# Kernel tuning notes

Measured on AMD Instinct MI355X. Metric: run time of the kernel, lower is better.

The kernel has to match this reference:

```python
import jax, jax.numpy as jnp
import numpy as np

EPS = 1e-06


def setup_inputs() -> dict:
    key = jax.random.key(0)
    k1, k2, k3 = jax.random.split(key, 3)
    B, L, S, C = 128, 512, 512, 64
    q = jax.random.normal(k1, (B, L, C), dtype=jnp.float32)
    k = jax.random.normal(k2, (B, S, C), dtype=jnp.float32)
    labels = jax.random.randint(k3, (B, L, S), 0, 2, dtype=jnp.int64)
    return {"q": q, "k": k, "labels": labels}


def reference(q, k, labels):
    # sim: [B, L, S], mapped to (0, 1) via (1 + cos-like sim) / 2
    sim = (1.0 + jnp.einsum('blc,bsc->bls', q, k)) * 0.5

    # column-wise stats (over L) -> [B, S]; torch.std uses ddof=1 (unbiased)
    col = (jnp.max(sim, axis=1) - jnp.mean(sim, axis=1)) / jnp.std(sim, axis=1, ddof=1)
    sharp1 = jax.nn.softmax(col, axis=-1)  # [B, S]

    # row-wise stats (over S) -> [B, L]
    row = (jnp.max(sim, axis=2) - jnp.mean(sim, axis=2)) / jnp.std(sim, axis=2, ddof=1)
    sharp2 = jax.nn.softmax(row, axis=-1)  # [B, L]

    simc = jnp.clip(sim, EPS, 1.0 - EPS)
    nll = -jnp.log(simc)                    # [B, L, S]
    nll_neg = -jnp.log(1.0 - simc)          # [B, L, S]

    pos = (labels == 1).astype(sim.dtype)
    neg = (labels == 0).astype(sim.dtype)

    # masked sums per sample, weighted by sharpness (broadcast over rows/cols)
    loss1 = jnp.sum(nll * sharp1[:, None, :] * pos, axis=(1, 2))  # [B]
    loss2 = jnp.sum(nll * sharp2[:, :, None] * pos, axis=(1, 2))  # [B]
    loss3 = jnp.sum(nll_neg * neg, axis=(1, 2)) / jnp.sum(neg, axis=(1, 2))  # [B]

    losses = (loss1 + loss2) * 0.5 + loss3
    return (sharp1, jnp.mean(losses))
```

## Files before the change

kernel.cpp:

```cpp
#include <hip/hip_runtime.h>

#define EPSF 1e-6f

typedef _Float16 half8 __attribute__((ext_vector_type(8)));
typedef float f32x4 __attribute__((ext_vector_type(4)));

constexpr int B = 128, L = 512, S = 512, C = 64;
constexpr int TILE_R = 64;
constexpr int TILES  = L / TILE_R;
constexpr int CHUNK  = 64;
constexpr int NCHUNK = S / CHUNK;

constexpr size_t WS_COLMAX = 0;
constexpr size_t WS_COLSUM = WS_COLMAX + (size_t)B * TILES * S;
constexpr size_t WS_COLSSQ = WS_COLSUM + (size_t)B * TILES * S;
constexpr size_t WS_COLP1  = WS_COLSSQ + (size_t)B * TILES * S;
constexpr size_t WS_ROWMAX = WS_COLP1  + (size_t)B * TILES * S;
constexpr size_t WS_ROWSUM = WS_ROWMAX + (size_t)B * L;
constexpr size_t WS_ROWSSQ = WS_ROWSUM + (size_t)B * L;
constexpr size_t WS_ROWP2  = WS_ROWSSQ + (size_t)B * L;
constexpr size_t WS_NEGS   = WS_ROWP2  + (size_t)B * L;
constexpr size_t WS_NEGC   = WS_NEGS   + (size_t)B * TILES;

__device__ inline void stageF(const float* __restrict__ g,
                              half8 (*__restrict__ hiA)[64],
                              half8 (*__restrict__ loA)[64], int t)
{
    const int row = t >> 2, c0 = (t & 3) * 16;
    const float* src = g + row * 64 + c0;
    float4 v0 = *(const float4*)(src);
    float4 v1 = *(const float4*)(src + 4);
    float4 v2 = *(const float4*)(src + 8);
    float4 v3 = *(const float4*)(src + 12);
    float v[16] = {v0.x, v0.y, v0.z, v0.w, v1.x, v1.y, v1.z, v1.w,
                   v2.x, v2.y, v2.z, v2.w, v3.x, v3.y, v3.z, v3.w};
#pragma unroll
    for (int o = 0; o < 2; ++o) {
        const int cb   = c0 + o * 8;
        const int idx  = (row >> 4) * 2 + (cb >> 5);
        const int lane_s = (((cb >> 3) & 3) << 4) + (row & 15);
        half8 h, l;
#pragma unroll
        for (int j = 0; j < 8; ++j) {
            float f = v[o * 8 + j];
            _Float16 hi = (_Float16)f;
            h[j] = hi;
            l[j] = (_Float16)(f - (float)hi);
        }
        hiA[idx][lane_s] = h;
        loA[idx][lane_s] = l;
    }
}

__global__ __launch_bounds__(256, 4)
void pass1_kernel(const float* __restrict__ q, const float* __restrict__ kmat,
                  const int* __restrict__ labels, float* __restrict__ ws)
{
    __shared__ half8 qhiF[8][64], qloF[8][64];
    __shared__ half8 khiF[8][64], kloF[8][64];
    __shared__ float4 colred4[4][CHUNK];
    __shared__ float nred[4][2];

    const int bidx = blockIdx.x;
    const int b    = bidx / TILES;
    const int tile = bidx % TILES;
    const int tid  = threadIdx.x;
    const int lane = tid & 63;
    const int wave = tid >> 6;
    const int l15  = lane & 15;
    const int quad = lane >> 4;
    const int rowbase = tile * TILE_R;

    float* colmax_p = ws + WS_COLMAX;
    float* colsum_p = ws + WS_COLSUM;
    float* colssq_p = ws + WS_COLSSQ;
    float* colp1_p  = ws + WS_COLP1;
    float* rowmax_p = ws + WS_ROWMAX;
    float* rowsum_p = ws + WS_ROWSUM;
    float* rowssq_p = ws + WS_ROWSSQ;
    float* rowp2_p  = ws + WS_ROWP2;
    float* negs_p   = ws + WS_NEGS;
    float* negc_p   = ws + WS_NEGC;

    stageF(q + ((size_t)b * L + rowbase) * C, qhiF, qloF, tid);

    float rmax[4], rsum[4], rssq[4], rp2[4];
#pragma unroll
    for (int i = 0; i < 4; ++i) { rmax[i] = -3.4e38f; rsum[i] = 0.f; rssq[i] = 0.f; rp2[i] = 0.f; }
    float negsum = 0.f, negcnt = 0.f;

    const float* kb = kmat + (size_t)b * S * C;
    const int*   lb = labels + ((size_t)b * L + rowbase) * S;

    for (int ch = 0; ch < NCHUNK; ++ch) {
        __syncthreads();
        stageF(kb + (size_t)ch * CHUNK * C, khiF, kloF, tid);
        __syncthreads();

        half8 ah0 = qhiF[wave * 2 + 0][lane], ah1 = qhiF[wave * 2 + 1][lane];
        half8 al0 = qloF[wave * 2 + 0][lane], al1 = qloF[wave * 2 + 1][lane];

        f32x4 acc[4];
#pragma unroll
        for (int ct = 0; ct < 4; ++ct) {
            half8 bh0 = khiF[ct * 2 + 0][lane], bh1 = khiF[ct * 2 + 1][lane];
            half8 bl0 = kloF[ct * 2 + 0][lane], bl1 = kloF[ct * 2 + 1][lane];
            f32x4 a = {0.f, 0.f, 0.f, 0.f};
            a = __builtin_amdgcn_mfma_f32_16x16x32_f16(ah0, bh0, a, 0, 0, 0);
            a = __builtin_amdgcn_mfma_f32_16x16x32_f16(ah0, bl0, a, 0, 0, 0);
            a = __builtin_amdgcn_mfma_f32_16x16x32_f16(al0, bh0, a, 0, 0, 0);
            a = __builtin_amdgcn_mfma_f32_16x16x32_f16(ah1, bh1, a, 0, 0, 0);
            a = __builtin_amdgcn_mfma_f32_16x16x32_f16(ah1, bl1, a, 0, 0, 0);
            a = __builtin_amdgcn_mfma_f32_16x16x32_f16(al1, bh1, a, 0, 0, 0);
            acc[ct] = a;
        }

        float cmax[4], csum[4], cssq[4], cp1[4];
#pragma unroll
        for (int ct = 0; ct < 4; ++ct) { cmax[ct] = -3.4e38f; csum[ct] = 0.f; cssq[ct] = 0.f; cp1[ct] = 0.f; }

#pragma unroll
        for (int ct = 0; ct < 4; ++ct) {
            const int colg = ch * CHUNK + ct * 16 + l15;
#pragma unroll
            for (int r = 0; r < 4; ++r) {
                const int rowl = wave * 16 + quad * 4 + r;
                int lab = lb[(size_t)rowl * S + colg];
                float sim = fmaf(0.5f, acc[ct][r], 0.5f);
                rmax[r] = fmaxf(rmax[r], sim);
                rsum[r] += sim;
                rssq[r] = fmaf(sim, sim, rssq[r]);
                cmax[ct] = fmaxf(cmax[ct], sim);
                csum[ct] += sim;
                cssq[ct] = fmaf(sim, sim, cssq[ct]);
                float sc  = fminf(fmaxf(sim, EPSF), 1.f - EPSF);
                bool  isp = (lab == 1);
                float pos = isp ? 1.f : 0.f;
                float t   = isp ? sc : (1.f - sc);
                float nl  = -__logf(t);
                float pn  = pos * nl;
                rp2[r] += pn;
                cp1[ct] += pn;
                negsum += nl - pn;
                negcnt += 1.f - pos;
            }
        }

#pragma unroll
        for (int ct = 0; ct < 4; ++ct) {
#pragma unroll
            for (int m = 16; m <= 32; m <<= 1) {
                cmax[ct] = fmaxf(cmax[ct], __shfl_xor(cmax[ct], m, 64));
                csum[ct] += __shfl_xor(csum[ct], m, 64);
                cssq[ct] += __shfl_xor(cssq[ct], m, 64);
                cp1[ct]  += __shfl_xor(cp1[ct],  m, 64);
            }
        }
        if (lane < 16) {
#pragma unroll
            for (int ct = 0; ct < 4; ++ct)
                colred4[wave][ct * 16 + l15] = make_float4(cmax[ct], csum[ct], cssq[ct], cp1[ct]);
        }
        __syncthreads();
        if (tid < CHUNK) {
            float4 v = colred4[0][tid];
            float m0 = v.x, s1 = v.y, s2 = v.z, pp = v.w;
#pragma unroll
            for (int w = 1; w < 4; ++w) {
                float4 u = colred4[w][tid];
                m0 = fmaxf(m0, u.x); s1 += u.y; s2 += u.z; pp += u.w;
            }
            size_t idx = ((size_t)b * TILES + tile) * S + ch * CHUNK + tid;
            colmax_p[idx] = m0; colsum_p[idx] = s1; colssq_p[idx] = s2; colp1_p[idx] = pp;
        }
    }

#pragma unroll
    for (int r = 0; r < 4; ++r) {
#pragma unroll
        for (int m = 1; m <= 8; m <<= 1) {
            rmax[r] = fmaxf(rmax[r], __shfl_xor(rmax[r], m, 64));
            rsum[r] += __shfl_xor(rsum[r], m, 64);
            rssq[r] += __shfl_xor(rssq[r], m, 64);
            rp2[r]  += __shfl_xor(rp2[r],  m, 64);
        }
    }
    if (l15 == 0) {
#pragma unroll
        for (int r = 0; r < 4; ++r) {
            size_t idx = (size_t)b * L + rowbase + wave * 16 + quad * 4 + r;
            rowmax_p[idx] = rmax[r]; rowsum_p[idx] = rsum[r];
            rowssq_p[idx] = rssq[r]; rowp2_p[idx]  = rp2[r];
        }
    }

#pragma unroll
    for (int m = 1; m <= 32; m <<= 1) {
        negsum += __shfl_xor(negsum, m, 64);
        negcnt += __shfl_xor(negcnt, m, 64);
    }
    if (lane == 0) { nred[wave][0] = negsum; nred[wave][1] = negcnt; }
    __syncthreads();
    if (tid == 0) {
        float ns = 0.f, nc = 0.f;
        for (int w = 0; w < 4; ++w) { ns += nred[w][0]; nc += nred[w][1]; }
        negs_p[bidx] = ns; negc_p[bidx] = nc;
    }
}

template <bool MAX>
__device__ inline float bred(float v, float* red)
{
#pragma unroll
    for (int m = 1; m <= 32; m <<= 1) {
        float o = __shfl_xor(v, m, 64);
        v = MAX ? fmaxf(v, o) : (v + o);
    }
    const int wave = threadIdx.x >> 6;
    const int lane = threadIdx.x & 63;
    if (lane == 0) red[wave] = v;
    __syncthreads();
    if (threadIdx.x == 0) {
        float r = red[0];
        for (int w = 1; w < 8; ++w) r = MAX ? fmaxf(r, red[w]) : (r + red[w]);
        red[8] = r;
    }
    __syncthreads();
    float out = red[8];
    __syncthreads();
    return out;
}

__global__ __launch_bounds__(512)
void pass2_kernel(const float* __restrict__ ws, float* __restrict__ out)
{
    __shared__ float red[9];
    const int b = blockIdx.x;
    const int s = threadIdx.x;

    if (blockIdx.y == 0) {
        const float* colmax_p = ws + WS_COLMAX;
        const float* colsum_p = ws + WS_COLSUM;
        const float* colssq_p = ws + WS_COLSSQ;
        const float* colp1_p  = ws + WS_COLP1;

        float m = -3.4e38f, sm = 0.f, sq = 0.f, p1 = 0.f;
#pragma unroll
        for (int t = 0; t < TILES; ++t) {
            size_t idx = ((size_t)b * TILES + t) * S + s;
            m = fmaxf(m, colmax_p[idx]);
            sm += colsum_p[idx];
            sq += colssq_p[idx];
            p1 += colp1_p[idx];
        }
        float mean  = sm * (1.f / L);
        float var   = (sq - sm * sm * (1.f / L)) * (1.f / (L - 1));
        float score = (m - mean) / sqrtf(var);

        float gmax = bred<true>(score, red);
        float e    = __expf(score - gmax);
        float esum = bred<false>(e, red);
        float sharp1 = e / esum;
        out[(size_t)b * S + s] = sharp1;
        float loss1 = bred<false>(sharp1 * p1, red);
        if (s == 0) atomicAdd(out + (size_t)B * S, loss1 * (0.5f / B));
    } else {
        const float* rowmax_p = ws + WS_ROWMAX;
        const float* rowsum_p = ws + WS_ROWSUM;
        const float* rowssq_p = ws + WS_ROWSSQ;
        const float* rowp2_p  = ws + WS_ROWP2;
        const float* negs_p   = ws + WS_NEGS;
        const float* negc_p   = ws + WS_NEGC;

        size_t ridx = (size_t)b * L + s;
        float m2 = rowmax_p[ridx], sm2 = rowsum_p[ridx];
        float sq2 = rowssq_p[ridx], p2 = rowp2_p[ridx];
        float mean2  = sm2 * (1.f / S);
        float var2   = (sq2 - sm2 * sm2 * (1.f / S)) * (1.f / (S - 1));
        float score2 = (m2 - mean2) / sqrtf(var2);

        float gmax2 = bred<true>(score2, red);
        float e2    = __expf(score2 - gmax2);
        float esum2 = bred<false>(e2, red);
        float loss2 = bred<false>((e2 / esum2) * p2, red);

        if (s == 0) {
            float ns = 0.f, nc = 0.f;
            for (int t = 0; t < TILES; ++t) { ns += negs_p[b * TILES + t]; nc += negc_p[b * TILES + t]; }
            atomicAdd(out + (size_t)B * S, (0.5f * loss2 + ns / nc) * (1.f / B));
        }
    }
}

extern "C" void kernel_launch(void* const* d_in, const int* in_sizes, int n_in,
                              void* d_out, int out_size, void* d_ws, size_t ws_size,
                              hipStream_t stream)
{
    const float* q      = (const float*)d_in[0];
    const float* k      = (const float*)d_in[1];
    const int*   labels = (const int*)d_in[2];
    float* out = (float*)d_out;
    float* ws  = (float*)d_ws;

    hipMemsetAsync((char*)d_out + (size_t)B * S * sizeof(float), 0, sizeof(float), stream);

    pass1_kernel<<<dim3(B * TILES), dim3(256), 0, stream>>>(q, k, labels, ws);
    pass2_kernel<<<dim3(B, 2), dim3(512), 0, stream>>>(ws, out);
}
```

Before: 274.5 us.

## Prefetch next K chunk in registers, hoist Q fragments, merge per-chunk barriers

```diff
diff --git a/kernel.cpp b/kernel.cpp
--- a/kernel.cpp
+++ b/kernel.cpp
@@ -22,22 +22,26 @@
 constexpr size_t WS_NEGS   = WS_ROWP2  + (size_t)B * L;
 constexpr size_t WS_NEGC   = WS_NEGS   + (size_t)B * TILES;
 
-__device__ inline void stageF(const float* __restrict__ g,
+__device__ inline void loadTile(const float* __restrict__ g, float4 v[4], int t)
+{
+    const float* src = g + (t >> 2) * 64 + (t & 3) * 16;
+    v[0] = *(const float4*)(src);
+    v[1] = *(const float4*)(src + 4);
+    v[2] = *(const float4*)(src + 8);
+    v[3] = *(const float4*)(src + 12);
+}
+
+__device__ inline void stageW(const float4 v4[4],
                               half8 (*__restrict__ hiA)[64],
                               half8 (*__restrict__ loA)[64], int t)
 {
     const int row = t >> 2, c0 = (t & 3) * 16;
-    const float* src = g + row * 64 + c0;
-    float4 v0 = *(const float4*)(src);
-    float4 v1 = *(const float4*)(src + 4);
-    float4 v2 = *(const float4*)(src + 8);
-    float4 v3 = *(const float4*)(src + 12);
-    float v[16] = {v0.x, v0.y, v0.z, v0.w, v1.x, v1.y, v1.z, v1.w,
-                   v2.x, v2.y, v2.z, v2.w, v3.x, v3.y, v3.z, v3.w};
+    const float v[16] = {v4[0].x, v4[0].y, v4[0].z, v4[0].w, v4[1].x, v4[1].y, v4[1].z, v4[1].w,
+                         v4[2].x, v4[2].y, v4[2].z, v4[2].w, v4[3].x, v4[3].y, v4[3].z, v4[3].w};
 #pragma unroll
     for (int o = 0; o < 2; ++o) {
-        const int cb   = c0 + o * 8;
-        const int idx  = (row >> 4) * 2 + (cb >> 5);
+        const int cb     = c0 + o * 8;
+        const int idx    = (row >> 4) * 2 + (cb >> 5);
         const int lane_s = (((cb >> 3) & 3) << 4) + (row & 15);
         half8 h, l;
 #pragma unroll
@@ -52,11 +56,10 @@
     }
 }
 
-__global__ __launch_bounds__(256, 4)
+__global__ __launch_bounds__(256, 5)
 void pass1_kernel(const float* __restrict__ q, const float* __restrict__ kmat,
                   const int* __restrict__ labels, float* __restrict__ ws)
 {
-    __shared__ half8 qhiF[8][64], qloF[8][64];
     __shared__ half8 khiF[8][64], kloF[8][64];
     __shared__ float4 colred4[4][CHUNK];
     __shared__ float nred[4][2];
@@ -82,23 +85,46 @@
     float* negs_p   = ws + WS_NEGS;
     float* negc_p   = ws + WS_NEGC;
 
-    stageF(q + ((size_t)b * L + rowbase) * C, qhiF, qloF, tid);
+    const float* kb = kmat + (size_t)b * S * C;
+    const int*   lb = labels + ((size_t)b * L + rowbase) * S;
+
+    float4 tv[4];
+    loadTile(q + ((size_t)b * L + rowbase) * C, tv, tid);
+    stageW(tv, khiF, kloF, tid);
+    half8 ah0 = khiF[wave * 2 + 0][lane], ah1 = khiF[wave * 2 + 1][lane];
+    half8 al0 = kloF[wave * 2 + 0][lane], al1 = kloF[wave * 2 + 1][lane];
+
+    loadTile(kb, tv, tid);
 
     float rmax[4], rsum[4], rssq[4], rp2[4];
 #pragma unroll
     for (int i = 0; i < 4; ++i) { rmax[i] = -3.4e38f; rsum[i] = 0.f; rssq[i] = 0.f; rp2[i] = 0.f; }
     float negsum = 0.f, negcnt = 0.f;
 
-    const float* kb = kmat + (size_t)b * S * C;
-    const int*   lb = labels + ((size_t)b * L + rowbase) * S;
-
     for (int ch = 0; ch < NCHUNK; ++ch) {
         __syncthreads();
-        stageF(kb + (size_t)ch * CHUNK * C, khiF, kloF, tid);
+        if (ch > 0 && tid < CHUNK) {
+            float4 v = colred4[0][tid];
+            float m0 = v.x, s1 = v.y, s2 = v.z, pp = v.w;
+#pragma unroll
+            for (int w = 1; w < 4; ++w) {
+                float4 u = colred4[w][tid];
+                m0 = fmaxf(m0, u.x); s1 += u.y; s2 += u.z; pp += u.w;
+            }
+            size_t idx = ((size_t)b * TILES + tile) * S + (ch - 1) * CHUNK + tid;
+            colmax_p[idx] = m0; colsum_p[idx] = s1; colssq_p[idx] = s2; colp1_p[idx] = pp;
+        }
+        stageW(tv, khiF, kloF, tid);
+        if (ch + 1 < NCHUNK)
+            loadTile(kb + (size_t)(ch + 1) * CHUNK * C, tv, tid);
         __syncthreads();
 
-        half8 ah0 = qhiF[wave * 2 + 0][lane], ah1 = qhiF[wave * 2 + 1][lane];
-        half8 al0 = qloF[wave * 2 + 0][lane], al1 = qloF[wave * 2 + 1][lane];
+        int labv[16];
+#pragma unroll
+        for (int ct = 0; ct < 4; ++ct)
+#pragma unroll
+            for (int r = 0; r < 4; ++r)
+                labv[ct * 4 + r] = lb[(size_t)(wave * 16 + quad * 4 + r) * S + ch * CHUNK + ct * 16 + l15];
 
         f32x4 acc[4];
 #pragma unroll
@@ -115,24 +141,19 @@
             acc[ct] = a;
         }
 
-        float cmax[4], csum[4], cssq[4], cp1[4];
-#pragma unroll
-        for (int ct = 0; ct < 4; ++ct) { cmax[ct] = -3.4e38f; csum[ct] = 0.f; cssq[ct] = 0.f; cp1[ct] = 0.f; }
-
 #pragma unroll
         for (int ct = 0; ct < 4; ++ct) {
-            const int colg = ch * CHUNK + ct * 16 + l15;
+            float cmax = -3.4e38f, csum = 0.f, cssq = 0.f, cp1 = 0.f;
 #pragma unroll
             for (int r = 0; r < 4; ++r) {
-                const int rowl = wave * 16 + quad * 4 + r;
-                int lab = lb[(size_t)rowl * S + colg];
+                int lab = labv[ct * 4 + r];
                 float sim = fmaf(0.5f, acc[ct][r], 0.5f);
                 rmax[r] = fmaxf(rmax[r], sim);
                 rsum[r] += sim;
                 rssq[r] = fmaf(sim, sim, rssq[r]);
-                cmax[ct] = fmaxf(cmax[ct], sim);
-                csum[ct] += sim;
-                cssq[ct] = fmaf(sim, sim, cssq[ct]);
+                cmax = fmaxf(cmax, sim);
+                csum += sim;
+                cssq = fmaf(sim, sim, cssq);
                 float sc  = fminf(fmaxf(sim, EPSF), 1.f - EPSF);
                 bool  isp = (lab == 1);
                 float pos = isp ? 1.f : 0.f;
@@ -140,39 +161,33 @@
                 float nl  = -__logf(t);
                 float pn  = pos * nl;
                 rp2[r] += pn;
-                cp1[ct] += pn;
+                cp1 += pn;
                 negsum += nl - pn;
                 negcnt += 1.f - pos;
             }
-        }
-
-#pragma unroll
-        for (int ct = 0; ct < 4; ++ct) {
 #pragma unroll
             for (int m = 16; m <= 32; m <<= 1) {
-                cmax[ct] = fmaxf(cmax[ct], __shfl_xor(cmax[ct], m, 64));
-                csum[ct] += __shfl_xor(csum[ct], m, 64);
-                cssq[ct] += __shfl_xor(cssq[ct], m, 64);
-                cp1[ct]  += __shfl_xor(cp1[ct],  m, 64);
+                cmax = fmaxf(cmax, __shfl_xor(cmax, m, 64));
+                csum += __shfl_xor(csum, m, 64);
+                cssq += __shfl_xor(cssq, m, 64);
+                cp1  += __shfl_xor(cp1,  m, 64);
             }
-        }
-        if (lane < 16) {
-#pragma unroll
-            for (int ct = 0; ct < 4; ++ct)
-                colred4[wave][ct * 16 + l15] = make_float4(cmax[ct], csum[ct], cssq[ct], cp1[ct]);
-        }
-        __syncthreads();
-        if (tid < CHUNK) {
-            float4 v = colred4[0][tid];
-            float m0 = v.x, s1 = v.y, s2 = v.z, pp = v.w;
-#pragma unroll
-            for (int w = 1; w < 4; ++w) {
-                float4 u = colred4[w][tid];
-                m0 = fmaxf(m0, u.x); s1 += u.y; s2 += u.z; pp += u.w;
-            }
-            size_t idx = ((size_t)b * TILES + tile) * S + ch * CHUNK + tid;
-            colmax_p[idx] = m0; colsum_p[idx] = s1; colssq_p[idx] = s2; colp1_p[idx] = pp;
-        }
+            if (lane < 16)
+                colred4[wave][ct * 16 + l15] = make_float4(cmax, csum, cssq, cp1);
+        }
+    }
+
+    __syncthreads();
+    if (tid < CHUNK) {
+        float4 v = colred4[0][tid];
+        float m0 = v.x, s1 = v.y, s2 = v.z, pp = v.w;
+#pragma unroll
+        for (int w = 1; w < 4; ++w) {
+            float4 u = colred4[w][tid];
+            m0 = fmaxf(m0, u.x); s1 += u.y; s2 += u.z; pp += u.w;
+        }
+        size_t idx = ((size_t)b * TILES + tile) * S + (NCHUNK - 1) * CHUNK + tid;
+        colmax_p[idx] = m0; colsum_p[idx] = s1; colssq_p[idx] = s2; colp1_p[idx] = pp;
     }
 
 #pragma unroll
```

Result: slower. 355.8 us (+29.6%).
